# Kernel optimization log

Measured on AMD Instinct MI355X. Metric: run time of the kernel, lower is better.

Reference implementation:

```python
import jax, jax.numpy as jnp
import numpy as np

IN_CH = 64
HID = 128


def skew(x):
    # [B,C,H,W] -> [B,C,H,H+W-1], row r shifted right by r
    B, C, H, W = x.shape
    rows = jnp.arange(H)[:, None]
    cols = rows + jnp.arange(W)[None, :]  # [H,W]
    out = jnp.zeros((B, C, H, H + W - 1), x.dtype)
    return out.at[:, :, rows, cols].set(x)


def unskew(x, W):
    B, C, H, _ = x.shape
    rows = jnp.arange(H)[:, None]
    cols = rows + jnp.arange(W)[None, :]
    return x[:, :, rows, cols]  # [B,C,H,W]


def setup_inputs() -> dict:
    key = jax.random.key(0)
    ks = jax.random.split(key, 7)
    B, C, H, W = 16, IN_CH, 64, 64
    s = 0.05
    return {
        "x": jax.random.normal(ks[0], (B, C, H, W), jnp.float32),
        "w_is": jax.random.normal(ks[1], (5 * HID, C), jnp.float32) * s,   # 1x1 conv (mask B @ k=1 is all-ones)
        "b_is": jax.random.normal(ks[2], (5 * HID,), jnp.float32) * s,
        "w_ss": jax.random.normal(ks[3], (5 * HID, HID, 2), jnp.float32) * s,  # Conv1d k=2
        "b_ss": jax.random.normal(ks[4], (5 * HID,), jnp.float32) * s,
        "w_res": jax.random.normal(ks[5], (HID, C), jnp.float32) * s,
        "b_res": jax.random.normal(ks[6], (HID,), jnp.float32) * s,
    }


def reference(x, w_is, b_is, w_ss, b_ss, w_res, b_res):
    B, C, H, W = x.shape
    skewed = skew(x)                                     # [B,C,H,SW]
    # input-to-state 1x1 conv over all skewed columns at once
    i_s = jnp.einsum('oc,bchw->bohw', w_is, skewed) + b_is[None, :, None, None]
    w0, w1 = w_ss[:, :, 0], w_ss[:, :, 1]                # taps: h_prev[t-1], h_prev[t]

    def step(carry, is_col):
        h_prev, c_prev = carry                           # [B,HID,H]
        hp_sh = jnp.pad(h_prev, ((0, 0), (0, 0), (1, 0)))[:, :, :-1]
        s_s = (jnp.einsum('oi,bih->boh', w0, hp_sh)
               + jnp.einsum('oi,bih->boh', w1, h_prev)
               + b_ss[None, :, None])
        gates = is_col + s_s                             # [B,5*HID,H]
        o, f_left, f_up, i, g = jnp.split(gates, 5, axis=1)
        o, f_left, f_up, i = map(jax.nn.sigmoid, (o, f_left, f_up, i))
        g = jnp.tanh(g)
        c_sh = jnp.pad(c_prev, ((0, 0), (0, 0), (1, 0)))[:, :, :-1]
        c = f_left * c_prev + f_up * c_sh + i * g
        h = o * jnp.tanh(c)                              # dropout = identity (eval)
        return (h, c), h

    h0 = jnp.zeros((B, HID, H), x.dtype)
    c0 = jnp.zeros((B, HID, H), x.dtype)
    is_cols = jnp.moveaxis(i_s, 3, 0)                    # [SW,B,5*HID,H]
    _, hs = jax.lax.scan(step, (h0, c0), is_cols)        # [SW,B,HID,H]
    total_h = unskew(jnp.moveaxis(hs, 0, 3), W)          # [B,HID,H,W]
    residual = jnp.einsum('oc,bchw->bohw', w_res, x) + b_res[None, :, None, None]
    return total_h + residual
```

## Files before the change

### kernel.cpp

```cpp
#include <hip/hip_runtime.h>


typedef __attribute__((ext_vector_type(4))) float f32x4;
typedef _Float16 half8 __attribute__((ext_vector_type(8)));

#define OFF_A1 0u
#define OFF_A2 327680u
#define OFF_V1 655360u
#define OFF_V2 737280u
#define OFF_SKEW 819200u
#define WS_NEED10 (819200u + 16777216u)
#define OFF_HA 17596416u
#define OFF_HB 25919488u
#define WS_NEED12 30081024u
#define OFF_XT 30081024u
#define WS_NEED13 46858240u

__device__ __forceinline__ float sgf(float x){ return 1.f / (1.f + __expf(-x)); }
__device__ __forceinline__ unsigned packsplit(float v){
  _Float16 a = (_Float16)v;
  _Float16 b = (_Float16)((v - (float)a) * 2048.f);
  unsigned short ua = *(unsigned short*)&a, ub = *(unsigned short*)&b;
  return ((unsigned)ub << 16) | ua;
}

__global__ void k0_prep(const float* __restrict__ w_is, const float* __restrict__ w_ss,
                        _Float16* __restrict__ A1, _Float16* __restrict__ A2,
                        _Float16* __restrict__ V1, _Float16* __restrict__ V2){
  int tid = blockIdx.x*blockDim.x + threadIdx.x;
  int nth = gridDim.x*blockDim.x;
  for (int idx = tid; idx < 163840; idx += nth){
    int e = idx & 7, l = (idx >> 3) & 63, ks = (idx >> 9) & 7, wv = (idx >> 12) & 7, gi = idx >> 15;
    int o = gi*128 + wv*16 + (l & 15);
    int k = ks*32 + ((l >> 4) << 3) + e;
    float v = (k < 128) ? w_ss[(size_t)(o*128 + k)*2] : w_ss[(size_t)(o*128 + (k-128))*2 + 1];
    _Float16 h1 = (_Float16)v;
    A1[idx] = h1;
    A2[idx] = (_Float16)((v - (float)h1) * 2048.f);
  }
  for (int idx = tid; idx < 40960; idx += nth){
    int e = idx & 7, l = (idx >> 3) & 63, ksx = (idx >> 9) & 1, wv = (idx >> 10) & 7, gi = idx >> 13;
    int o = gi*128 + wv*16 + (l & 15);
    int kx = ksx*32 + ((l >> 4) << 3) + e;
    float v = w_is[o*64 + kx];
    _Float16 h1 = (_Float16)v;
    V1[idx] = h1;
    V2[idx] = (_Float16)((v - (float)h1) * 2048.f);
  }
}

__global__ __launch_bounds__(256) void k1_xt(const float* __restrict__ x,
                                             unsigned* __restrict__ xT){
  __shared__ unsigned tl[64*65];
  int b = blockIdx.x >> 6, r = blockIdx.x & 63;
  for (int idx = threadIdx.x; idx < 4096; idx += 256){
    int cp = idx >> 6, c = idx & 63;
    tl[cp*65 + c] = packsplit(x[(size_t)(b*64 + cp)*4096 + r*64 + c]);
  }
  __syncthreads();
  for (int idx = threadIdx.x; idx < 4096; idx += 256){
    int c = idx >> 6, cp = idx & 63;
    xT[(size_t)((b*64 + r)*64 + c)*64 + cp] = tl[cp*65 + c];
  }
}

__global__ __launch_bounds__(256) void k_res(const float* __restrict__ x,
      const float* __restrict__ w_res, const float* __restrict__ b_res,
      float* __restrict__ out){
  __shared__ float xt[64*65];
  __shared__ float wl[128*64];
  __shared__ float bl[128];
  int b = blockIdx.x >> 6, r = blockIdx.x & 63;
  int tid = threadIdx.x;
  for (int idx = tid; idx < 4096; idx += 256){
    int cp = idx >> 6, c = idx & 63;
    xt[cp*65 + c] = x[(size_t)(b*64 + cp)*4096 + r*64 + c];
  }
  for (int idx = tid; idx < 8192; idx += 256) wl[idx] = w_res[idx];
  if (tid < 128) bl[tid] = b_res[tid];
  __syncthreads();
  int c = tid & 63, chg = tid >> 6;
  float xcol[64];
  #pragma unroll
  for (int cp = 0; cp < 64; ++cp) xcol[cp] = xt[cp*65 + c];
  for (int ch = chg*32; ch < chg*32 + 32; ++ch){
    float acc = bl[ch];
    const float* wrow = &wl[ch*64];
    #pragma unroll
    for (int cp = 0; cp < 64; cp += 4){
      float4 w4 = *(const float4*)&wrow[cp];
      acc += w4.x*xcol[cp] + w4.y*xcol[cp+1] + w4.z*xcol[cp+2] + w4.w*xcol[cp+3];
    }
    out[(size_t)((b*128 + ch)*64 + r)*64 + c] = acc;
  }
}

template<int XMODE>
__global__ __launch_bounds__(512) void k2_par(const _Float16* __restrict__ A1,
      const _Float16* __restrict__ A2, const _Float16* __restrict__ V1,
      const _Float16* __restrict__ V2, const float* __restrict__ x,
      const unsigned* __restrict__ xT,
      const float* __restrict__ b_is, const float* __restrict__ b_ss,
      _Float16* __restrict__ skewh, unsigned long long* __restrict__ HA,
      unsigned* __restrict__ HB){
  __shared__ __align__(16) _Float16 h1l[17][136];
  __shared__ __align__(16) _Float16 h2l[17][136];
  __shared__ __align__(16) float clds[128][18];
  __shared__ __align__(16) _Float16 x1l[2][16][72];
  __shared__ __align__(16) _Float16 x2l[2][16][72];
  __shared__ __align__(16) float blds[640];
  __shared__ unsigned bh[128];
  __shared__ float bc[128];
  int blk = blockIdx.x, b = blk >> 2, g = blk & 3;
  int r0 = g << 4;
  int tid = threadIdx.x, wv = tid >> 6, l = tid & 63, rl = l & 15, kg = l >> 4;
  int ch0 = wv*16 + kg*4;
  const float* xb = x + (size_t)b*262144;
  const unsigned* xTb = xT + (size_t)b*262144;
  const half8* A1f = (const half8*)A1;
  const half8* A2f = (const half8*)A2;
  const half8* V1f = (const half8*)V1;
  const half8* V2f = (const half8*)V2;
  const float INV2048 = 1.f/2048.f;

  for (int i2 = tid; i2 < 17*136; i2 += 512){
    ((_Float16*)h1l)[i2] = (_Float16)0.f;
    ((_Float16*)h2l)[i2] = (_Float16)0.f;
  }
  for (int i2 = tid; i2 < 128*18; i2 += 512) ((float*)clds)[i2] = 0.f;
  for (int i2 = tid; i2 < 640; i2 += 512) blds[i2] = b_is[i2] + b_ss[i2];
  for (int idx = tid; idx < 1024; idx += 512){
    int rr = idx >> 6, cp = idx & 63;
    int c = 0 - (r0 + rr);
    unsigned u;
    if (XMODE == 1){
      u = (((unsigned)c) < 64u) ? xTb[((r0 + rr)*64 + c)*64 + cp] : 0u;
    } else {
      float v = (((unsigned)c) < 64u) ? xb[cp*4096 + (r0 + rr)*64 + c] : 0.f;
      u = packsplit(v);
    }
    unsigned short s1 = (unsigned short)(u & 0xffffu), s2 = (unsigned short)(u >> 16);
    x1l[0][rr][cp] = *(_Float16*)&s1;
    x2l[0][rr][cp] = *(_Float16*)&s2;
  }
  __syncthreads();

  #pragma unroll 1
  for (int t = 0; t < 127; ++t){
    unsigned xs[2];
    #pragma unroll
    for (int q = 0; q < 2; ++q){
      int idx = tid + (q << 9);
      int rr = idx >> 6, cp = idx & 63;
      int c = t + 1 - (r0 + rr);
      if (XMODE == 1){
        xs[q] = (((unsigned)c) < 64u) ? xTb[((r0 + rr)*64 + c)*64 + cp] : 0u;
      } else {
        float v = (((unsigned)c) < 64u) ? xb[cp*4096 + (r0 + rr)*64 + c] : 0.f;
        xs[q] = packsplit(v);
      }
    }
    int xslot = t & 1;

    f32x4 am[5], ac[5];
    #pragma unroll
    for (int gi = 0; gi < 5; ++gi){
      am[gi] = *(const f32x4*)&blds[gi*128 + ch0];
      ac[gi] = (f32x4){0.f,0.f,0.f,0.f};
    }
    half8 wa1[2][5], wa2[2][5];
    #pragma unroll
    for (int gi = 0; gi < 5; ++gi){
      wa1[0][gi] = A1f[((gi*8 + wv)*8 + 0)*64 + l];
      wa2[0][gi] = A2f[((gi*8 + wv)*8 + 0)*64 + l];
    }
    #pragma unroll
    for (int ks = 0; ks < 10; ++ks){
      const int cur = ks & 1, nxt = cur ^ 1;
      if (ks < 9){
        const int kn = ks + 1;
        #pragma unroll
        for (int gi = 0; gi < 5; ++gi){
          if (kn < 8){
            wa1[nxt][gi] = A1f[((gi*8 + wv)*8 + kn)*64 + l];
            wa2[nxt][gi] = A2f[((gi*8 + wv)*8 + kn)*64 + l];
          } else {
            wa1[nxt][gi] = V1f[((gi*8 + wv)*2 + (kn - 8))*64 + l];
            wa2[nxt][gi] = V2f[((gi*8 + wv)*2 + (kn - 8))*64 + l];
          }
        }
      }
      half8 B1, B2;
      if (ks < 8){
        int ri = (ks < 4) ? rl : (rl + 1);
        int col = (ks & 3)*32 + kg*8;
        B1 = *(const half8*)&h1l[ri][col];
        B2 = *(const half8*)&h2l[ri][col];
      } else {
        int col = (ks - 8)*32 + kg*8;
        B1 = *(const half8*)&x1l[xslot][rl][col];
        B2 = *(const half8*)&x2l[xslot][rl][col];
      }
      #pragma unroll
      for (int gi = 0; gi < 5; ++gi){
        am[gi] = __builtin_amdgcn_mfma_f32_16x16x32_f16(wa1[cur][gi], B1, am[gi], 0, 0, 0);
        ac[gi] = __builtin_amdgcn_mfma_f32_16x16x32_f16(wa1[cur][gi], B2, ac[gi], 0, 0, 0);
        ac[gi] = __builtin_amdgcn_mfma_f32_16x16x32_f16(wa2[cur][gi], B1, ac[gi], 0, 0, 0);
      }
    }
    int r = r0 + rl;
    int cc = t - r;
    bool vld = ((unsigned)cc) < 64u;
    float cn_s[4]; _Float16 h1_s[4], h2_s[4];
    #pragma unroll
    for (int j = 0; j < 4; ++j){
      int ch = ch0 + j;
      float g0 = am[0][j] + ac[0][j]*INV2048;
      float g1 = am[1][j] + ac[1][j]*INV2048;
      float g2 = am[2][j] + ac[2][j]*INV2048;
      float g3 = am[3][j] + ac[3][j]*INV2048;
      float g4 = am[4][j] + ac[4][j]*INV2048;
      float ccur = clds[ch][rl + 1];
      float clft = clds[ch][rl];
      float og = sgf(g0), fl = sgf(g1), fu = sgf(g2), ii = sgf(g3);
      float gg = tanhf(g4);
      float cn = fl*ccur + fu*clft + ii*gg;
      float hv = og * tanhf(cn);
      cn_s[j] = cn;
      _Float16 hh = (_Float16)hv;
      h1_s[j] = hh;
      h2_s[j] = (_Float16)((hv - (float)hh) * 2048.f);
    }
    __syncthreads();

    #pragma unroll
    for (int j = 0; j < 4; ++j) clds[ch0 + j][rl + 1] = cn_s[j];
    union { _Float16 h[4]; uint2 u; unsigned long long w; } u1, u2;
    #pragma unroll
    for (int j = 0; j < 4; ++j){ u1.h[j] = h1_s[j]; u2.h[j] = h2_s[j]; }
    *(uint2*)&h1l[rl + 1][ch0] = u1.u;
    *(uint2*)&h2l[rl + 1][ch0] = u2.u;
    if (vld)
      __builtin_nontemporal_store(u1.w,
          (unsigned long long*)&skewh[(((size_t)(b*64 + r)*64 + cc) << 7) + ch0]);
    if (g < 3 && t < 126 && rl == 15){
      #pragma unroll
      for (int j = 0; j < 4; ++j){
        unsigned hb1 = *(unsigned short*)&h1_s[j];
        unsigned hb2 = *(unsigned short*)&h2_s[j];
        bh[ch0 + j] = (hb2 << 16) | hb1;
        bc[ch0 + j] = cn_s[j];
      }
    }
    #pragma unroll
    for (int q = 0; q < 2; ++q){
      int idx = tid + (q << 9);
      int rr = idx >> 6, cp = idx & 63;
      unsigned u = xs[q];
      unsigned short s1 = (unsigned short)(u & 0xffffu), s2 = (unsigned short)(u >> 16);
      x1l[xslot ^ 1][rr][cp] = *(_Float16*)&s1;
      x2l[xslot ^ 1][rr][cp] = *(_Float16*)&s2;
    }
    __syncthreads();

    if (t < 126){
      if (g < 3 && tid < 128){
        size_t e = ((size_t)(b*4 + g)*127 + t)*128 + tid;
        __hip_atomic_store(&HB[e], __float_as_uint(bc[tid]),
                           __ATOMIC_RELAXED, __HIP_MEMORY_SCOPE_AGENT);
        unsigned long long a = (((unsigned long long)(t + 1)) << 32)
                             | (unsigned long long)bh[tid];
        __hip_atomic_store(&HA[e], a,
                           __ATOMIC_RELEASE, __HIP_MEMORY_SCOPE_AGENT);
      }
      if (g > 0 && tid < 128){
        size_t e2 = ((size_t)(b*4 + g - 1)*127 + t)*128 + tid;
        unsigned long long a;
        for (;;){
          a = __hip_atomic_load(&HA[e2], __ATOMIC_RELAXED, __HIP_MEMORY_SCOPE_AGENT);
          if ((unsigned)(a >> 32) == (unsigned)(t + 1)) break;
          __builtin_amdgcn_s_sleep(1);
        }
        a = __hip_atomic_load(&HA[e2], __ATOMIC_ACQUIRE, __HIP_MEMORY_SCOPE_AGENT);
        unsigned cb = __hip_atomic_load(&HB[e2], __ATOMIC_RELAXED, __HIP_MEMORY_SCOPE_AGENT);
        unsigned hx = (unsigned)a;
        unsigned short hh1 = (unsigned short)(hx & 0xffffu);
        unsigned short hh2 = (unsigned short)(hx >> 16);
        *(unsigned short*)&h1l[0][tid] = hh1;
        *(unsigned short*)&h2l[0][tid] = hh2;
        clds[tid][0] = __uint_as_float(cb);
      }
      __syncthreads();
    }
  }
}

template<int MODE>
__global__ __launch_bounds__(512) void k2_rec(const _Float16* __restrict__ A1,
      const _Float16* __restrict__ A2, const _Float16* __restrict__ V1,
      const _Float16* __restrict__ V2, const float* __restrict__ x,
      const float* __restrict__ b_is, const float* __restrict__ b_ss,
      _Float16* __restrict__ skewh, float* __restrict__ out){
  __shared__ __align__(16) _Float16 h1l[65][136];
  __shared__ __align__(16) _Float16 h2l[65][136];
  __shared__ __align__(16) float clds[128][66];
  __shared__ __align__(16) _Float16 x1l[2][64][72];
  __shared__ __align__(16) _Float16 x2l[2][64][72];
  __shared__ __align__(16) float blds[640];
  int b = blockIdx.x, tid = threadIdx.x;
  int wv = tid >> 6, l = tid & 63, rl = l & 15, kg = l >> 4;
  int ch0 = wv*16 + kg*4;
  const float* xb = x + (size_t)b*262144;
  const half8* A1f = (const half8*)A1;
  const half8* A2f = (const half8*)A2;
  const half8* V1f = (const half8*)V1;
  const half8* V2f = (const half8*)V2;

  for (int i2 = tid; i2 < 65*136; i2 += 512){ ((_Float16*)h1l)[i2] = (_Float16)0.f; ((_Float16*)h2l)[i2] = (_Float16)0.f; }
  for (int i2 = tid; i2 < 128*66; i2 += 512) ((float*)clds)[i2] = 0.f;
  for (int i2 = tid; i2 < 640; i2 += 512) blds[i2] = b_is[i2] + b_ss[i2];
  for (int idx = tid; idx < 4096; idx += 512){
    int cp = idx >> 6, r = idx & 63;
    int c = 0 - r;
    float v = (((unsigned)c) < 64u) ? xb[cp*4096 + r*64 + c] : 0.f;
    _Float16 a = (_Float16)v;
    x1l[0][r][cp] = a;
    x2l[0][r][cp] = (_Float16)((v - (float)a) * 2048.f);
  }
  __syncthreads();

  float cn_s[2][4]; _Float16 h1_s[2][4], h2_s[2][4]; float ov_s[2][4]; int vld_s[2];
  const float INV2048 = 1.f/2048.f;

  auto process = [&](int mtb, int t, int xslot){
    float rv[2][4];
    if (MODE == 1){
      #pragma unroll
      for (int m2 = 0; m2 < 2; ++m2){
        int r = ((mtb + m2) << 4) + rl;
        int c = t - r;
        bool valid = ((unsigned)c) < 64u;
        #pragma unroll
        for (int j = 0; j < 4; ++j)
          rv[m2][j] = valid ? out[(size_t)((b*128 + ch0 + j)*64 + r)*64 + c] : 0.f;
      }
    }
    f32x4 am[5][2], ac[5][2];
    #pragma unroll
    for (int gi = 0; gi < 5; ++gi){
      f32x4 bv = *(const f32x4*)&blds[gi*128 + ch0];
      am[gi][0] = bv; am[gi][1] = bv;
      ac[gi][0] = (f32x4){0.f,0.f,0.f,0.f};
      ac[gi][1] = (f32x4){0.f,0.f,0.f,0.f};
    }
    half8 wa1[2][5], wa2[2][5];
    #pragma unroll
    for (int gi = 0; gi < 5; ++gi){
      wa1[0][gi] = A1f[((gi*8 + wv)*8 + 0)*64 + l];
      wa2[0][gi] = A2f[((gi*8 + wv)*8 + 0)*64 + l];
    }
    #pragma unroll
    for (int ks = 0; ks < 10; ++ks){
      const int cur = ks & 1, nxt = cur ^ 1;
      if (ks < 9){
        const int kn = ks + 1;
        #pragma unroll
        for (int gi = 0; gi < 5; ++gi){
          if (kn < 8){
            wa1[nxt][gi] = A1f[((gi*8 + wv)*8 + kn)*64 + l];
            wa2[nxt][gi] = A2f[((gi*8 + wv)*8 + kn)*64 + l];
          } else {
            wa1[nxt][gi] = V1f[((gi*8 + wv)*2 + (kn - 8))*64 + l];
            wa2[nxt][gi] = V2f[((gi*8 + wv)*2 + (kn - 8))*64 + l];
          }
        }
      }
      half8 B1[2], B2[2];
      #pragma unroll
      for (int m2 = 0; m2 < 2; ++m2){
        int r = ((mtb + m2) << 4) + rl;
        if (ks < 8){
          int ri = (ks < 4) ? r : (r + 1);
          int col = (ks & 3)*32 + kg*8;
          B1[m2] = *(const half8*)&h1l[ri][col];
          B2[m2] = *(const half8*)&h2l[ri][col];
        } else {
          int col = (ks - 8)*32 + kg*8;
          B1[m2] = *(const half8*)&x1l[xslot][r][col];
          B2[m2] = *(const half8*)&x2l[xslot][r][col];
        }
      }
      #pragma unroll
      for (int gi = 0; gi < 5; ++gi){
        #pragma unroll
        for (int m2 = 0; m2 < 2; ++m2){
          am[gi][m2] = __builtin_amdgcn_mfma_f32_16x16x32_f16(wa1[cur][gi], B1[m2], am[gi][m2], 0, 0, 0);
          ac[gi][m2] = __builtin_amdgcn_mfma_f32_16x16x32_f16(wa1[cur][gi], B2[m2], ac[gi][m2], 0, 0, 0);
          ac[gi][m2] = __builtin_amdgcn_mfma_f32_16x16x32_f16(wa2[cur][gi], B1[m2], ac[gi][m2], 0, 0, 0);
        }
      }
    }
    #pragma unroll
    for (int m2 = 0; m2 < 2; ++m2){
      int r = ((mtb + m2) << 4) + rl;
      int c = t - r;
      vld_s[m2] = ((unsigned)c) < 64u;
      #pragma unroll
      for (int j = 0; j < 4; ++j){
        int ch = ch0 + j;
        float g0 = am[0][m2][j] + ac[0][m2][j]*INV2048;
        float g1 = am[1][m2][j] + ac[1][m2][j]*INV2048;
        float g2 = am[2][m2][j] + ac[2][m2][j]*INV2048;
        float g3 = am[3][m2][j] + ac[3][m2][j]*INV2048;
        float g4 = am[4][m2][j] + ac[4][m2][j]*INV2048;
        float ccur = clds[ch][r];
        float clft = (r == 0) ? 0.f : clds[ch][r - 1];
        float og = sgf(g0), fl = sgf(g1), fu = sgf(g2), ii = sgf(g3);
        float gg = tanhf(g4);
        float cn = fl*ccur + fu*clft + ii*gg;
        float hv = og * tanhf(cn);
        cn_s[m2][j] = cn;
        _Float16 hh = (_Float16)hv;
        h1_s[m2][j] = hh;
        h2_s[m2][j] = (_Float16)((hv - (float)hh) * 2048.f);
        if (MODE == 1) ov_s[m2][j] = rv[m2][j] + hv;
      }
    }
  };

  auto commit = [&](int mtb, int t){
    #pragma unroll
    for (int m2 = 0; m2 < 2; ++m2){
      int r = ((mtb + m2) << 4) + rl;
      #pragma unroll
      for (int j = 0; j < 4; ++j) clds[ch0 + j][r] = cn_s[m2][j];
      union { _Float16 h[4]; uint2 u; } u1, u2;
      #pragma unroll
      for (int j = 0; j < 4; ++j){ u1.h[j] = h1_s[m2][j]; u2.h[j] = h2_s[m2][j]; }
      *(uint2*)&h1l[r + 1][ch0] = u1.u;
      *(uint2*)&h2l[r + 1][ch0] = u2.u;
      if (vld_s[m2]){
        int c = t - r;
        if (MODE == 0){
          *(uint2*)&skewh[(((size_t)(b*64 + r)*64 + c) << 7) + ch0] = u1.u;
        } else {
          #pragma unroll
          for (int j = 0; j < 4; ++j)
            out[(size_t)((b*128 + ch0 + j)*64 + r)*64 + c] = ov_s[m2][j];
        }
      }
    }
  };

  #pragma unroll 1
  for (int t = 0; t < 127; ++t){
    float xs[8];
    #pragma unroll
    for (int q = 0; q < 8; ++q){
      int idx = tid + (q << 9);
      int cp = idx >> 6, r = idx & 63;
      int c = t + 1 - r;
      xs[q] = (((unsigned)c) < 64u) ? xb[cp*4096 + r*64 + c] : 0.f;
    }
    int xslot = t & 1;
    process(2, t, xslot);
    __syncthreads();
    commit(2, t);
    process(0, t, xslot);
    __syncthreads();
    commit(0, t);
    #pragma unroll
    for (int q = 0; q < 8; ++q){
      int idx = tid + (q << 9);
      int cp = idx >> 6, r = idx & 63;
      float v = xs[q];
      _Float16 a = (_Float16)v;
      x1l[xslot ^ 1][r][cp] = a;
      x2l[xslot ^ 1][r][cp] = (_Float16)((v - (float)a) * 2048.f);
    }
    __syncthreads();
  }
}

__global__ __launch_bounds__(256) void k3_merge(const _Float16* __restrict__ skewh,
                                                float* __restrict__ out){
  __shared__ _Float16 hl[64*134];
  int b = blockIdx.x >> 6, r = blockIdx.x & 63;
  const _Float16* src = skewh + ((size_t)(b*64 + r) << 13);
  for (int idx = threadIdx.x; idx < 8192; idx += 256)
    hl[(idx >> 7)*134 + (idx & 127)] = src[idx];
  __syncthreads();
  int c = threadIdx.x & 63, chg = threadIdx.x >> 6;
  for (int ch = chg*32; ch < chg*32 + 32; ++ch){
    size_t oi = ((size_t)(b*128 + ch)*64 + r)*64 + c;
    out[oi] += (float)hl[c*134 + ch];
  }
}

extern "C" void kernel_launch(void* const* d_in, const int* in_sizes, int n_in,
                              void* d_out, int out_size, void* d_ws, size_t ws_size,
                              hipStream_t stream){
  const float* x     = (const float*)d_in[0];
  const float* w_is  = (const float*)d_in[1];
  const float* b_is  = (const float*)d_in[2];
  const float* w_ss  = (const float*)d_in[3];
  const float* b_ss  = (const float*)d_in[4];
  const float* w_res = (const float*)d_in[5];
  const float* b_res = (const float*)d_in[6];
  float* out = (float*)d_out;
  char* ws = (char*)d_ws;
  _Float16* A1 = (_Float16*)(ws + OFF_A1);
  _Float16* A2 = (_Float16*)(ws + OFF_A2);
  _Float16* V1 = (_Float16*)(ws + OFF_V1);
  _Float16* V2 = (_Float16*)(ws + OFF_V2);
  _Float16* SK = (_Float16*)(ws + OFF_SKEW);

  hipLaunchKernelGGL(k0_prep, dim3(8), dim3(256), 0, stream,
                     w_is, w_ss, A1, A2, V1, V2);
  hipLaunchKernelGGL(k_res, dim3(1024), dim3(256), 0, stream,
                     x, w_res, b_res, out);
  if (ws_size >= (size_t)WS_NEED13){
    unsigned long long* HA = (unsigned long long*)(ws + OFF_HA);
    unsigned* HB           = (unsigned*)(ws + OFF_HB);
    unsigned* XT           = (unsigned*)(ws + OFF_XT);
    hipLaunchKernelGGL(k1_xt, dim3(1024), dim3(256), 0, stream, x, XT);
    hipLaunchKernelGGL((k2_par<1>), dim3(64), dim3(512), 0, stream,
                       A1, A2, V1, V2, x, XT, b_is, b_ss, SK, HA, HB);
    hipLaunchKernelGGL(k3_merge, dim3(1024), dim3(256), 0, stream, SK, out);
  } else if (ws_size >= (size_t)WS_NEED12){
    unsigned long long* HA = (unsigned long long*)(ws + OFF_HA);
    unsigned* HB           = (unsigned*)(ws + OFF_HB);
    hipLaunchKernelGGL((k2_par<0>), dim3(64), dim3(512), 0, stream,
                       A1, A2, V1, V2, x, (const unsigned*)nullptr, b_is, b_ss, SK, HA, HB);
    hipLaunchKernelGGL(k3_merge, dim3(1024), dim3(256), 0, stream, SK, out);
  } else if (ws_size >= (size_t)WS_NEED10){
    hipLaunchKernelGGL((k2_rec<0>), dim3(16), dim3(512), 0, stream,
                       A1, A2, V1, V2, x, b_is, b_ss, SK, out);
    hipLaunchKernelGGL(k3_merge, dim3(1024), dim3(256), 0, stream, SK, out);
  } else {
    hipLaunchKernelGGL((k2_rec<1>), dim3(16), dim3(512), 0, stream,
                       A1, A2, V1, V2, x, b_is, b_ss, (_Float16*)nullptr, out);
  }
}
```

Before: 2.459 ms.

## Batch inter-block hidden-state handoff into 8-step epochs with LDS ring buffer

Replaces the per-step release/acquire spin handshake between neighbouring row-group blocks with an epoch counter. The counter is published every 8 steps. The consumer block waits once per epoch, then prefetches 8 steps of boundary h/c values into a shared-memory ring and reads from it on each step. This is meant to cut the number of cross-block polling round trips on the recurrence critical path. The cost is that each downstream block must now lag its predecessor by up to 8 steps, which lengthens the pipeline fill across the 4 row groups.

```diff
diff --git a/kernel.cpp b/kernel.cpp
--- a/kernel.cpp
+++ b/kernel.cpp
@@ -111,6 +111,7 @@
   __shared__ __align__(16) float blds[640];
   __shared__ unsigned bh[128];
   __shared__ float bc[128];
+  __shared__ uint2 ring[8][128];
   int blk = blockIdx.x, b = blk >> 2, g = blk & 3;
   int r0 = g << 4;
   int tid = threadIdx.x, wv = tid >> 6, l = tid & 63, rl = l & 15, kg = l >> 4;
@@ -122,6 +123,7 @@
   const half8* V1f = (const half8*)V1;
   const half8* V2f = (const half8*)V2;
   const float INV2048 = 1.f/2048.f;
+  unsigned long long* EPa = HA + ((size_t)(b*4 + 3) * 127) * 128;
 
   for (int i2 = tid; i2 < 17*136; i2 += 512){
     ((_Float16*)h1l)[i2] = (_Float16)0.f;
@@ -271,24 +273,55 @@
         unsigned long long a = (((unsigned long long)(t + 1)) << 32)
                              | (unsigned long long)bh[tid];
         __hip_atomic_store(&HA[e], a,
-                           __ATOMIC_RELEASE, __HIP_MEMORY_SCOPE_AGENT);
-      }
-      if (g > 0 && tid < 128){
-        size_t e2 = ((size_t)(b*4 + g - 1)*127 + t)*128 + tid;
-        unsigned long long a;
-        for (;;){
-          a = __hip_atomic_load(&HA[e2], __ATOMIC_RELAXED, __HIP_MEMORY_SCOPE_AGENT);
-          if ((unsigned)(a >> 32) == (unsigned)(t + 1)) break;
-          __builtin_amdgcn_s_sleep(1);
-        }
-        a = __hip_atomic_load(&HA[e2], __ATOMIC_ACQUIRE, __HIP_MEMORY_SCOPE_AGENT);
-        unsigned cb = __hip_atomic_load(&HB[e2], __ATOMIC_RELAXED, __HIP_MEMORY_SCOPE_AGENT);
-        unsigned hx = (unsigned)a;
-        unsigned short hh1 = (unsigned short)(hx & 0xffffu);
-        unsigned short hh2 = (unsigned short)(hx >> 16);
-        *(unsigned short*)&h1l[0][tid] = hh1;
-        *(unsigned short*)&h2l[0][tid] = hh2;
-        clds[tid][0] = __uint_as_float(cb);
+                           __ATOMIC_RELAXED, __HIP_MEMORY_SCOPE_AGENT);
+      }
+      bool estep = (((t + 1) & 7) == 0) || (t == 125);
+      if (estep){
+        __syncthreads();
+        if (g < 3 && tid == 0)
+          __hip_atomic_store(&EPa[g], (unsigned long long)(t + 1),
+                             __ATOMIC_RELEASE, __HIP_MEMORY_SCOPE_AGENT);
+      }
+      if (g > 0){
+        if ((t & 7) == 0){
+          unsigned long long need = (unsigned long long)((t + 8 < 126) ? (t + 8) : 126);
+          if (tid == 0){
+            for (;;){
+              unsigned long long v = __hip_atomic_load(&EPa[g - 1],
+                                  __ATOMIC_RELAXED, __HIP_MEMORY_SCOPE_AGENT);
+              if (v >= need && v <= 126ull) break;
+              __builtin_amdgcn_s_sleep(2);
+            }
+            (void)__hip_atomic_load(&EPa[g - 1],
+                                  __ATOMIC_ACQUIRE, __HIP_MEMORY_SCOPE_AGENT);
+          }
+          __syncthreads();
+          if (tid < 128){
+            #pragma unroll
+            for (int j = 0; j < 8; ++j){
+              int tg = t + 1 + j;
+              if (tg <= 126){
+                size_t e2 = ((size_t)(b*4 + g - 1)*127 + (tg - 1))*128 + tid;
+                unsigned long long a;
+                for (;;){
+                  a = __hip_atomic_load(&HA[e2], __ATOMIC_RELAXED, __HIP_MEMORY_SCOPE_AGENT);
+                  if ((unsigned)(a >> 32) == (unsigned)tg) break;
+                  __builtin_amdgcn_s_sleep(1);
+                }
+                unsigned cb = __hip_atomic_load(&HB[e2], __ATOMIC_RELAXED, __HIP_MEMORY_SCOPE_AGENT);
+                uint2 rv; rv.x = (unsigned)a; rv.y = cb;
+                ring[tg & 7][tid] = rv;
+              }
+            }
+          }
+        }
+        if (tid < 128){
+          uint2 rv = ring[(t + 1) & 7][tid];
+          unsigned hx = rv.x;
+          *(unsigned short*)&h1l[0][tid] = (unsigned short)(hx & 0xffffu);
+          *(unsigned short*)&h2l[0][tid] = (unsigned short)(hx >> 16);
+          clds[tid][0] = __uint_as_float(rv.y);
+        }
       }
       __syncthreads();
     }
```

After: 2.825 ms. 14.9% more time.
